# Optimization experiments

Hardware: AMD Instinct MI355X
Metric: run time of the kernel (lower is better)

The kernel has to match this reference:

```python
import jax, jax.numpy as jnp
import numpy as np
from jax import lax

B, C_IN, C_OUT, H, W = 8, 64, 64, 256, 256
C_RED = max(1, C_OUT // 8)
THETA = 0.7


def setup_inputs() -> dict:
    key = jax.random.key(0)
    ks = jax.random.split(key, 8)
    s = 0.05
    return {
        "x": jax.random.normal(ks[0], (B, C_IN, H, W), dtype=jnp.float32),
        "W_conv": jax.random.normal(ks[1], (C_OUT, C_IN, 3, 3), dtype=jnp.float32) * s,
        "b_conv": jax.random.normal(ks[2], (C_OUT,), dtype=jnp.float32) * s,
        "W_edge": jax.random.normal(ks[3], (C_OUT, C_IN), dtype=jnp.float32) * s,
        "W_att1": jax.random.normal(ks[4], (C_RED, C_OUT), dtype=jnp.float32) * s,
        "b_att1": jax.random.normal(ks[5], (C_RED,), dtype=jnp.float32) * s,
        "W_att2": jax.random.normal(ks[6], (C_OUT, C_RED), dtype=jnp.float32) * s,
        "b_att2": jax.random.normal(ks[7], (C_OUT,), dtype=jnp.float32) * s,
    }


def reference(x, W_conv, b_conv, W_edge, W_att1, b_att1, W_att2, b_att2):
    # main 3x3 conv, stride 1, padding 1
    conv_out = lax.conv_general_dilated(
        x, W_conv, window_strides=(1, 1), padding=((1, 1), (1, 1)),
        dimension_numbers=("NCHW", "OIHW", "NCHW"))
    conv_out = conv_out + b_conv[None, :, None, None]

    # diff_v: the (C,C,3,3) diagonal kernel is exactly a per-channel vertical
    # shift-difference: out(y) = x(y-1) - x(y+1) with zero padding.
    xp = jnp.pad(x, ((0, 0), (0, 0), (1, 1), (0, 0)))
    diff_v = xp[:, :, :-2, :] - xp[:, :, 2:, :]  # [B, C, H, W]

    # 1x1 edge conv on |diff_v| (no bias)
    edge_out = jnp.einsum("oc,bchw->bohw", W_edge, jnp.abs(diff_v))

    combined = THETA * conv_out + (1.0 - THETA) * edge_out

    # SE attention: GAP -> 1x1 -> ReLU -> 1x1 -> sigmoid
    pooled = combined.mean(axis=(2, 3))                      # [B, C]
    h = jax.nn.relu(pooled @ W_att1.T + b_att1)              # [B, C//8]
    attn = jax.nn.sigmoid(h @ W_att2.T + b_att2)             # [B, C]

    return combined * attn[:, :, None, None]
```

## Files before the change

kernel.cpp:

```cpp
#include <hip/hip_runtime.h>
#include <hip/hip_bf16.h>
#include <math.h>

#define THETA 0.7f

typedef short short8 __attribute__((ext_vector_type(8)));
typedef float floatx4 __attribute__((ext_vector_type(4)));

__device__ __forceinline__ unsigned short f2bu(float f) {
    return __builtin_bit_cast(unsigned short, __float2bfloat16(f));
}
__device__ __forceinline__ float b2f(unsigned short u) {
    unsigned v = ((unsigned)u) << 16;
    return __builtin_bit_cast(float, v);
}

__global__ void cdc_prep(const float* __restrict__ Wc,
                         const float* __restrict__ We,
                         unsigned short* __restrict__ Bw)
{
    int idx = blockIdx.x * 256 + threadIdx.x;
    if (idx >= 2 * 64 * 328) return;
    int k = idx % 328;
    int n = (idx / 328) & 63;
    int chunk = idx / 20992;
    int c0 = chunk << 5;
    float v = 0.f;
    if (k < 288) {
        int tap = k >> 5, cl = k & 31;
        v = THETA * Wc[n * 576 + (c0 + cl) * 9 + tap];
    } else if (k < 320) {
        int cl = k - 288;
        v = (1.0f - THETA) * We[n * 64 + c0 + cl];
    }
    Bw[idx] = f2bu(v);
}

__global__ __launch_bounds__(256, 2) void cdc_main_kernel(
    const float* __restrict__ x, const unsigned short* __restrict__ Bw,
    const float* __restrict__ bc, float* __restrict__ out,
    float* __restrict__ sums)
{
    __shared__ unsigned short xs[18 * 22 * 40];
    __shared__ unsigned short bs[64 * 328];

    const int tid  = threadIdx.x;
    const int lane = tid & 63;
    const int w    = tid >> 6;
    const int m    = lane & 15;
    const int q    = lane >> 4;

    const int tile = blockIdx.x;
    const int b    = tile >> 8;
    const int trow = ((tile >> 4) & 15) << 4;
    const int tcol = (tile & 15) << 4;

    floatx4 acc[4][4];
    #pragma unroll
    for (int nf = 0; nf < 4; ++nf) {
        float bias = THETA * bc[nf * 16 + m];
        #pragma unroll
        for (int mf = 0; mf < 4; ++mf)
            acc[mf][nf] = (floatx4){bias, bias, bias, bias};
    }

    for (int chunk = 0; chunk < 2; ++chunk) {
        const int c0 = chunk << 5;
        __syncthreads();
        {
            const ulonglong2* src = (const ulonglong2*)(Bw + chunk * 20992);
            ulonglong2* dst = (ulonglong2*)bs;
            for (int i = tid; i < 2624; i += 256) dst[i] = src[i];
        }
        for (int bi = tid; bi < 720; bi += 256) {
            const int cgrp = bi / 90;
            const int rem  = bi - cgrp * 90;
            const int row  = rem / 5;
            const int cg   = rem - row * 5;
            const int gr   = trow + row - 1;
            const int gc0  = tcol + (cg << 2) - 1;
            float v[4][4];
            const bool rok = (unsigned)gr < 256u;
            const float* xb = x + (((size_t)(b * 64 + c0 + cgrp * 4)) * 256 +
                                   (rok ? gr : 0)) * 256;
            if (rok && gc0 >= 0 && gc0 + 3 < 256) {
                #pragma unroll
                for (int i = 0; i < 4; ++i) {
                    float4 t = *(const float4*)(xb + (size_t)i * 65536 + gc0);
                    v[i][0] = t.x; v[i][1] = t.y; v[i][2] = t.z; v[i][3] = t.w;
                }
            } else {
                #pragma unroll
                for (int i = 0; i < 4; ++i)
                    #pragma unroll
                    for (int e = 0; e < 4; ++e) {
                        int gc = gc0 + e;
                        v[i][e] = (rok && (unsigned)gc < 256u)
                                  ? xb[(size_t)i * 65536 + gc] : 0.f;
                    }
            }
            unsigned short* dst = &xs[(row * 22 + (cg << 2)) * 40 + (cgrp << 2)];
            #pragma unroll
            for (int e = 0; e < 4; ++e) {
                unsigned long long d =
                      (unsigned long long)f2bu(v[0][e])
                    | ((unsigned long long)f2bu(v[1][e]) << 16)
                    | ((unsigned long long)f2bu(v[2][e]) << 32)
                    | ((unsigned long long)f2bu(v[3][e]) << 48);
                *(unsigned long long*)(dst + e * 40) = d;
            }
        }
        __syncthreads();

        #pragma unroll
        for (int tap = 0; tap < 9; ++tap) {
            const int dy = tap / 3, dx = tap % 3;
            short8 bf[4];
            #pragma unroll
            for (int nf = 0; nf < 4; ++nf)
                bf[nf] = *(const short8*)
                    &bs[(nf * 16 + m) * 328 + tap * 32 + q * 8];
            #pragma unroll
            for (int mf = 0; mf < 4; ++mf) {
                const short8 af = *(const short8*)
                    &xs[((w * 4 + mf + dy) * 22 + (m + dx)) * 40 + q * 8];
                #pragma unroll
                for (int nf = 0; nf < 4; ++nf)
                    acc[mf][nf] = __builtin_amdgcn_mfma_f32_16x16x32_bf16(
                        af, bf[nf], acc[mf][nf], 0, 0, 0);
            }
        }
        {
            short8 bf[4];
            #pragma unroll
            for (int nf = 0; nf < 4; ++nf)
                bf[nf] = *(const short8*)&bs[(nf * 16 + m) * 328 + 288 + q * 8];
            #pragma unroll
            for (int mf = 0; mf < 4; ++mf) {
                const short8 a0 = *(const short8*)
                    &xs[((w * 4 + mf) * 22 + m + 1) * 40 + q * 8];
                const short8 a1 = *(const short8*)
                    &xs[((w * 4 + mf + 2) * 22 + m + 1) * 40 + q * 8];
                short8 af;
                #pragma unroll
                for (int j = 0; j < 8; ++j)
                    af[j] = (short)f2bu(fabsf(
                        b2f((unsigned short)a0[j]) - b2f((unsigned short)a1[j])));
                #pragma unroll
                for (int nf = 0; nf < 4; ++nf)
                    acc[mf][nf] = __builtin_amdgcn_mfma_f32_16x16x32_bf16(
                        af, bf[nf], acc[mf][nf], 0, 0, 0);
            }
        }
    }

    #pragma unroll
    for (int mf = 0; mf < 4; ++mf) {
        const int y = trow + w * 4 + mf;
        #pragma unroll
        for (int nf = 0; nf < 4; ++nf) {
            const int oc = nf * 16 + m;
            size_t off = (((size_t)(b * 64 + oc)) * 256 + y) * 256 + tcol + q * 4;
            float4 val = make_float4(acc[mf][nf][0], acc[mf][nf][1],
                                     acc[mf][nf][2], acc[mf][nf][3]);
            *(float4*)(out + off) = val;
        }
    }

    float p[4];
    #pragma unroll
    for (int nf = 0; nf < 4; ++nf) {
        float s = 0.f;
        #pragma unroll
        for (int mf = 0; mf < 4; ++mf)
            s += acc[mf][nf][0] + acc[mf][nf][1] + acc[mf][nf][2] + acc[mf][nf][3];
        s += __shfl_xor(s, 32);
        s += __shfl_xor(s, 16);
        p[nf] = s;
    }
    __syncthreads();
    float* red = (float*)xs;
    if (q == 0) {
        #pragma unroll
        for (int nf = 0; nf < 4; ++nf) red[w * 64 + nf * 16 + m] = p[nf];
    }
    __syncthreads();
    if (tid < 64) {
        float s = red[tid] + red[64 + tid] + red[128 + tid] + red[192 + tid];
        atomicAdd(&sums[b * 64 + tid], s);
    }
}

__global__ __launch_bounds__(64) void cdc_attn_kernel(
    const float* __restrict__ sums,
    const float* __restrict__ W1, const float* __restrict__ b1,
    const float* __restrict__ W2, const float* __restrict__ b2,
    float* __restrict__ attn)
{
    __shared__ float pooled[512];
    __shared__ float hbuf[64];
    const int tid = threadIdx.x;
    const float inv = 1.0f / 65536.0f;
    for (int i = tid; i < 512; i += 64) pooled[i] = sums[i] * inv;
    __syncthreads();
    {
        int bb = tid >> 3, r = tid & 7;
        float s = b1[r];
        for (int o = 0; o < 64; ++o) s += W1[r * 64 + o] * pooled[bb * 64 + o];
        hbuf[bb * 8 + r] = fmaxf(s, 0.f);
    }
    __syncthreads();
    {
        int o = tid;
        for (int bb = 0; bb < 8; ++bb) {
            float z = b2[o];
            #pragma unroll
            for (int r = 0; r < 8; ++r) z += W2[o * 8 + r] * hbuf[bb * 8 + r];
            attn[bb * 64 + o] = 1.0f / (1.0f + expf(-z));
        }
    }
}

__global__ __launch_bounds__(256) void cdc_scale_kernel(
    float* __restrict__ out, const float* __restrict__ attn)
{
    int i = blockIdx.x * 256 + threadIdx.x;
    float4* o4 = reinterpret_cast<float4*>(out);
    float4 v = o4[i];
    float a = attn[i >> 14];
    v.x *= a; v.y *= a; v.z *= a; v.w *= a;
    o4[i] = v;
}

extern "C" void kernel_launch(void* const* d_in, const int* in_sizes, int n_in,
                              void* d_out, int out_size, void* d_ws, size_t ws_size,
                              hipStream_t stream)
{
    const float* x  = (const float*)d_in[0];
    const float* Wc = (const float*)d_in[1];
    const float* bc = (const float*)d_in[2];
    const float* We = (const float*)d_in[3];
    const float* W1 = (const float*)d_in[4];
    const float* b1 = (const float*)d_in[5];
    const float* W2 = (const float*)d_in[6];
    const float* b2 = (const float*)d_in[7];
    float* out  = (float*)d_out;

    float* sums = (float*)d_ws;
    float* attn = sums + 512;
    unsigned short* Bw = (unsigned short*)(attn + 512);

    hipMemsetAsync(sums, 0, 512 * sizeof(float), stream);
    cdc_prep<<<164, 256, 0, stream>>>(Wc, We, Bw);
    cdc_main_kernel<<<2048, 256, 0, stream>>>(x, Bw, bc, out, sums);
    cdc_attn_kernel<<<1, 64, 0, stream>>>(sums, W1, b1, W2, b2, attn);
    cdc_scale_kernel<<<32768, 256, 0, stream>>>(out, attn);
}
```

Before: 357.1 us.

## Compute SE pooling analytically from input statistics, fuse attention scaling into conv epilogue

```diff
diff --git a/kernel.cpp b/kernel.cpp
--- a/kernel.cpp
+++ b/kernel.cpp
@@ -14,16 +14,21 @@
     unsigned v = ((unsigned)u) << 16;
     return __builtin_bit_cast(float, v);
 }
+__device__ __forceinline__ float wsum64(float v) {
+    v += __shfl_xor(v, 32); v += __shfl_xor(v, 16); v += __shfl_xor(v, 8);
+    v += __shfl_xor(v, 4);  v += __shfl_xor(v, 2);  v += __shfl_xor(v, 1);
+    return v;
+}
 
 __global__ void cdc_prep(const float* __restrict__ Wc,
                          const float* __restrict__ We,
                          unsigned short* __restrict__ Bw)
 {
     int idx = blockIdx.x * 256 + threadIdx.x;
-    if (idx >= 2 * 64 * 328) return;
-    int k = idx % 328;
-    int n = (idx / 328) & 63;
-    int chunk = idx / 20992;
+    if (idx >= 2 * 64 * 384) return;
+    int k = idx % 384;
+    int n = (idx / 384) & 63;
+    int chunk = idx / 24576;
     int c0 = chunk << 5;
     float v = 0.f;
     if (k < 288) {
@@ -36,13 +41,130 @@
     Bw[idx] = f2bu(v);
 }
 
-__global__ __launch_bounds__(256, 2) void cdc_main_kernel(
+__global__ __launch_bounds__(1024) void cdc_stats(
+    const float* __restrict__ x, float* __restrict__ stats)
+{
+    __shared__ float rT[16], rD[16], rR0[4], rR255[4], rC0[4], rC255[4], rCorn[4];
+    const int tid  = threadIdx.x;
+    const int j    = tid & 255;
+    const int seg  = tid >> 8;
+    const int w    = tid >> 6;
+    const int lane = tid & 63;
+    const float* p = x + (size_t)blockIdx.x * 65536 + j;
+
+    const int r0 = seg << 6;
+    float colsum = 0.f, D = 0.f;
+    float xm = (r0 == 0) ? 0.f : p[(size_t)(r0 - 1) * 256];
+    float xc = p[(size_t)r0 * 256];
+    const float x_first = xc;
+    float x_last = 0.f;
+    #pragma unroll 8
+    for (int r = r0; r < r0 + 64; ++r) {
+        float xp = (r + 1 < 256) ? p[(size_t)(r + 1) * 256] : 0.f;
+        colsum += xc;
+        D += fabsf(xm - xp);
+        if (r == r0 + 63) x_last = xc;
+        xm = xc; xc = xp;
+    }
+
+    float ts = wsum64(colsum);
+    float ds = wsum64(D);
+    if (lane == 0) { rT[w] = ts; rD[w] = ds; }
+    if (seg == 0) {
+        float fs = wsum64(x_first);
+        if (lane == 0) rR0[w] = fs;
+    } else if (seg == 3) {
+        float fs = wsum64(x_last);
+        if (lane == 0) rR255[w & 3] = fs;
+    }
+    if (j == 0) {
+        rC0[seg] = colsum;
+        if (seg == 0) rCorn[0] = x_first;
+        if (seg == 3) rCorn[2] = x_last;
+    }
+    if (j == 255) {
+        rC255[seg] = colsum;
+        if (seg == 0) rCorn[1] = x_first;
+        if (seg == 3) rCorn[3] = x_last;
+    }
+    __syncthreads();
+    if (tid == 0) {
+        float T = 0.f, Dt = 0.f;
+        #pragma unroll
+        for (int i = 0; i < 16; ++i) { T += rT[i]; Dt += rD[i]; }
+        float* st = stats + (size_t)blockIdx.x * 10;
+        st[0] = T;
+        st[1] = rR0[0] + rR0[1] + rR0[2] + rR0[3];
+        st[2] = rR255[0] + rR255[1] + rR255[2] + rR255[3];
+        st[3] = rC0[0] + rC0[1] + rC0[2] + rC0[3];
+        st[4] = rC255[0] + rC255[1] + rC255[2] + rC255[3];
+        st[5] = rCorn[0]; st[6] = rCorn[1]; st[7] = rCorn[2]; st[8] = rCorn[3];
+        st[9] = Dt;
+    }
+}
+
+__global__ __launch_bounds__(256) void cdc_attn(
+    const float* __restrict__ stats, const float* __restrict__ Wc,
+    const float* __restrict__ bc, const float* __restrict__ We,
+    const float* __restrict__ W1, const float* __restrict__ b1,
+    const float* __restrict__ W2, const float* __restrict__ b2,
+    float* __restrict__ attn)
+{
+    __shared__ float S9[512][9];
+    __shared__ float Dl[512];
+    __shared__ float pooled[512];
+    __shared__ float hb[64];
+    const int tid = threadIdx.x;
+    for (int i = tid; i < 512; i += 256) {
+        const float* st = stats + (size_t)i * 10;
+        float T = st[0], R0 = st[1], R255 = st[2], C0 = st[3], C255 = st[4];
+        float Rex[3]  = {R255, 0.f, R0};
+        float Cex[3]  = {C255, 0.f, C0};
+        float corn[9] = {st[8], 0.f, st[7],
+                         0.f,   0.f, 0.f,
+                         st[6], 0.f, st[5]};
+        #pragma unroll
+        for (int tap = 0; tap < 9; ++tap)
+            S9[i][tap] = T - Rex[tap / 3] - Cex[tap % 3] + corn[tap];
+        Dl[i] = st[9];
+    }
+    __syncthreads();
+    for (int i = tid; i < 512; i += 256) {
+        int b = i >> 6, o = i & 63;
+        float cs = 0.f, es = 0.f;
+        for (int c = 0; c < 64; ++c) {
+            const float* wp = Wc + o * 576 + c * 9;
+            const float* sp = S9[b * 64 + c];
+            #pragma unroll
+            for (int tap = 0; tap < 9; ++tap) cs += wp[tap] * sp[tap];
+            es += We[o * 64 + c] * Dl[b * 64 + c];
+        }
+        pooled[i] = THETA * (cs * (1.f / 65536.f) + bc[o])
+                  + (1.0f - THETA) * (es * (1.f / 65536.f));
+    }
+    __syncthreads();
+    if (tid < 64) {
+        int b = tid >> 3, r = tid & 7;
+        float s = b1[r];
+        for (int o = 0; o < 64; ++o) s += W1[r * 64 + o] * pooled[b * 64 + o];
+        hb[tid] = fmaxf(s, 0.f);
+    }
+    __syncthreads();
+    for (int i = tid; i < 512; i += 256) {
+        int b = i >> 6, o = i & 63;
+        float z = b2[o];
+        #pragma unroll
+        for (int r = 0; r < 8; ++r) z += W2[o * 8 + r] * hb[b * 8 + r];
+        attn[i] = 1.0f / (1.0f + expf(-z));
+    }
+}
+
+__global__ __launch_bounds__(256, 4) void cdc_main_kernel(
     const float* __restrict__ x, const unsigned short* __restrict__ Bw,
-    const float* __restrict__ bc, float* __restrict__ out,
-    float* __restrict__ sums)
+    const float* __restrict__ bc, const float* __restrict__ attn,
+    float* __restrict__ out)
 {
     __shared__ unsigned short xs[18 * 22 * 40];
-    __shared__ unsigned short bs[64 * 328];
 
     const int tid  = threadIdx.x;
     const int lane = tid & 63;
@@ -50,10 +172,14 @@
     const int m    = lane & 15;
     const int q    = lane >> 4;
 
-    const int tile = blockIdx.x;
-    const int b    = tile >> 8;
-    const int trow = ((tile >> 4) & 15) << 4;
-    const int tcol = (tile & 15) << 4;
+    int wg = (int)blockIdx.x;
+    wg = ((wg & 7) << 8) | (wg >> 3);
+    const int b    = wg >> 8;
+    const int t    = wg & 255;
+    const int trow = ((t >> 4) & 15) << 4;
+    const int tcol = (t & 15) << 4;
+
+    const unsigned short* Bl = Bw + m * 384 + q * 8;
 
     floatx4 acc[4][4];
     #pragma unroll
@@ -66,12 +192,8 @@
 
     for (int chunk = 0; chunk < 2; ++chunk) {
         const int c0 = chunk << 5;
+        const unsigned short* Bc = Bl + chunk * 24576;
         __syncthreads();
-        {
-            const ulonglong2* src = (const ulonglong2*)(Bw + chunk * 20992);
-            ulonglong2* dst = (ulonglong2*)bs;
-            for (int i = tid; i < 2624; i += 256) dst[i] = src[i];
-        }
         for (int bi = tid; bi < 720; bi += 256) {
             const int cgrp = bi / 90;
             const int rem  = bi - cgrp * 90;
@@ -86,8 +208,8 @@
             if (rok && gc0 >= 0 && gc0 + 3 < 256) {
                 #pragma unroll
                 for (int i = 0; i < 4; ++i) {
-                    float4 t = *(const float4*)(xb + (size_t)i * 65536 + gc0);
-                    v[i][0] = t.x; v[i][1] = t.y; v[i][2] = t.z; v[i][3] = t.w;
+                    float4 tv = *(const float4*)(xb + (size_t)i * 65536 + gc0);
+                    v[i][0] = tv.x; v[i][1] = tv.y; v[i][2] = tv.z; v[i][3] = tv.w;
                 }
             } else {
                 #pragma unroll
@@ -118,8 +240,7 @@
             short8 bf[4];
             #pragma unroll
             for (int nf = 0; nf < 4; ++nf)
-                bf[nf] = *(const short8*)
-                    &bs[(nf * 16 + m) * 328 + tap * 32 + q * 8];
+                bf[nf] = *(const short8*)&Bc[nf * 6144 + tap * 32];
             #pragma unroll
             for (int mf = 0; mf < 4; ++mf) {
                 const short8 af = *(const short8*)
@@ -134,7 +255,7 @@
             short8 bf[4];
             #pragma unroll
             for (int nf = 0; nf < 4; ++nf)
-                bf[nf] = *(const short8*)&bs[(nf * 16 + m) * 328 + 288 + q * 8];
+                bf[nf] = *(const short8*)&Bc[nf * 6144 + 288];
             #pragma unroll
             for (int mf = 0; mf < 4; ++mf) {
                 const short8 a0 = *(const short8*)
@@ -143,9 +264,9 @@
                     &xs[((w * 4 + mf + 2) * 22 + m + 1) * 40 + q * 8];
                 short8 af;
                 #pragma unroll
-                for (int j = 0; j < 8; ++j)
-                    af[j] = (short)f2bu(fabsf(
-                        b2f((unsigned short)a0[j]) - b2f((unsigned short)a1[j])));
+                for (int jj = 0; jj < 8; ++jj)
+                    af[jj] = (short)f2bu(fabsf(
+                        b2f((unsigned short)a0[jj]) - b2f((unsigned short)a1[jj])));
                 #pragma unroll
                 for (int nf = 0; nf < 4; ++nf)
                     acc[mf][nf] = __builtin_amdgcn_mfma_f32_16x16x32_bf16(
@@ -154,6 +275,9 @@
         }
     }
 
+    float av[4];
+    #pragma unroll
+    for (int nf = 0; nf < 4; ++nf) av[nf] = attn[b * 64 + nf * 16 + m];
     #pragma unroll
     for (int mf = 0; mf < 4; ++mf) {
         const int y = trow + w * 4 + mf;
@@ -161,75 +285,13 @@
         for (int nf = 0; nf < 4; ++nf) {
             const int oc = nf * 16 + m;
             size_t off = (((size_t)(b * 64 + oc)) * 256 + y) * 256 + tcol + q * 4;
-            float4 val = make_float4(acc[mf][nf][0], acc[mf][nf][1],
-                                     acc[mf][nf][2], acc[mf][nf][3]);
+            float4 val = make_float4(acc[mf][nf][0] * av[nf],
+                                     acc[mf][nf][1] * av[nf],
+                                     acc[mf][nf][2] * av[nf],
+                                     acc[mf][nf][3] * av[nf]);
             *(float4*)(out + off) = val;
         }
     }
-
-    float p[4];
-    #pragma unroll
-    for (int nf = 0; nf < 4; ++nf) {
-        float s = 0.f;
-        #pragma unroll
-        for (int mf = 0; mf < 4; ++mf)
-            s += acc[mf][nf][0] + acc[mf][nf][1] + acc[mf][nf][2] + acc[mf][nf][3];
-        s += __shfl_xor(s, 32);
-        s += __shfl_xor(s, 16);
-        p[nf] = s;
-    }
-    __syncthreads();
-    float* red = (float*)xs;
-    if (q == 0) {
-        #pragma unroll
-        for (int nf = 0; nf < 4; ++nf) red[w * 64 + nf * 16 + m] = p[nf];
-    }
-    __syncthreads();
-    if (tid < 64) {
-        float s = red[tid] + red[64 + tid] + red[128 + tid] + red[192 + tid];
-        atomicAdd(&sums[b * 64 + tid], s);
-    }
-}
-
-__global__ __launch_bounds__(64) void cdc_attn_kernel(
-    const float* __restrict__ sums,
-    const float* __restrict__ W1, const float* __restrict__ b1,
-    const float* __restrict__ W2, const float* __restrict__ b2,
-    float* __restrict__ attn)
-{
-    __shared__ float pooled[512];
-    __shared__ float hbuf[64];
-    const int tid = threadIdx.x;
-    const float inv = 1.0f / 65536.0f;
-    for (int i = tid; i < 512; i += 64) pooled[i] = sums[i] * inv;
-    __syncthreads();
-    {
-        int bb = tid >> 3, r = tid & 7;
-        float s = b1[r];
-        for (int o = 0; o < 64; ++o) s += W1[r * 64 + o] * pooled[bb * 64 + o];
-        hbuf[bb * 8 + r] = fmaxf(s, 0.f);
-    }
-    __syncthreads();
-    {
-        int o = tid;
-        for (int bb = 0; bb < 8; ++bb) {
-            float z = b2[o];
-            #pragma unroll
-            for (int r = 0; r < 8; ++r) z += W2[o * 8 + r] * hbuf[bb * 8 + r];
-            attn[bb * 64 + o] = 1.0f / (1.0f + expf(-z));
-        }
-    }
-}
-
-__global__ __launch_bounds__(256) void cdc_scale_kernel(
-    float* __restrict__ out, const float* __restrict__ attn)
-{
-    int i = blockIdx.x * 256 + threadIdx.x;
-    float4* o4 = reinterpret_cast<float4*>(out);
-    float4 v = o4[i];
-    float a = attn[i >> 14];
-    v.x *= a; v.y *= a; v.z *= a; v.w *= a;
-    o4[i] = v;
 }
 
 extern "C" void kernel_launch(void* const* d_in, const int* in_sizes, int n_in,
@@ -246,13 +308,12 @@
     const float* b2 = (const float*)d_in[7];
     float* out  = (float*)d_out;
 
-    float* sums = (float*)d_ws;
-    float* attn = sums + 512;
+    float* stats = (float*)d_ws;
+    float* attn  = stats + 5120;
     unsigned short* Bw = (unsigned short*)(attn + 512);
 
-    hipMemsetAsync(sums, 0, 512 * sizeof(float), stream);
-    cdc_prep<<<164, 256, 0, stream>>>(Wc, We, Bw);
-    cdc_main_kernel<<<2048, 256, 0, stream>>>(x, Bw, bc, out, sums);
-    cdc_attn_kernel<<<1, 64, 0, stream>>>(sums, W1, b1, W2, b2, attn);
-    cdc_scale_kernel<<<32768, 256, 0, stream>>>(out, attn);
-}
+    cdc_prep<<<192, 256, 0, stream>>>(Wc, We, Bw);
+    cdc_stats<<<512, 1024, 0, stream>>>(x, stats);
+    cdc_attn<<<1, 256, 0, stream>>>(stats, Wc, bc, We, W1, b1, W2, b2, attn);
+    cdc_main_kernel<<<2048, 256, 0, stream>>>(x, Bw, bc, attn, out);
+}
```

After: 454.3 us. +27.2%, slower.
